# Kernel tuning notes

Hardware: AMD Instinct MI355X
Metric: run time of the kernel (lower is better)

Reference implementation:

```python
import jax, jax.numpy as jnp
import numpy as np

DIM = 8
H1 = 128
H2 = 128
BATCH = 65536


def setup_inputs() -> dict:
    key = jax.random.key(0)
    ks = jax.random.split(key, 9)
    s = lambda k, shape, scale: jax.random.normal(k, shape, dtype=jnp.float32) * scale
    return {
        "X": s(ks[0], (BATCH, 2 * DIM), 1.0),
        "K": s(ks[1], (DIM, DIM), 0.5),
        "D": s(ks[2], (DIM, DIM), 0.5),
        "W0": s(ks[3], (H1, DIM), 1.0 / np.sqrt(DIM)),
        "b0": s(ks[4], (H1,), 0.1),
        "W1": s(ks[5], (H2, H1), 1.0 / np.sqrt(H1)),
        "b1": s(ks[6], (H2,), 0.1),
        "W2": s(ks[7], (1, H2), 1.0 / np.sqrt(H2)),
        "b2": s(ks[8], (1,), 0.1),
    }


def reference(X, K, D, W0, b0, W1, b1, W2, b2):
    dim = K.shape[0]
    x = X[:, :dim]   # position  [B, d]
    v = X[:, dim:]   # velocity  [B, d]

    # Embedding height function f: R^d -> R (MLP with tanh), y = [x, f(x)]
    def f_scalar(xi):
        h = jnp.tanh(W0 @ xi + b0)
        h = jnp.tanh(W1 @ h + b1)
        return (W2 @ h + b2)[0]

    g = jax.vmap(jax.grad(f_scalar))(x)      # grad f   [B, d]
    H = jax.vmap(jax.hessian(f_scalar))(x)   # hess f   [B, d, d]

    eye = jnp.eye(dim, dtype=X.dtype)
    m = eye + g[:, :, None] * g[:, None, :]  # metric I + g g^T  [B, d, d]
    minv = jnp.linalg.inv(m)                 # batched inverse   [B, d, d]

    # linear part: m^{-1} ( -(D v + K x) )
    force = -(v @ D.T + x @ K.T)                      # [B, d]
    lin = jnp.einsum('bqk,bk->bq', minv, force)       # [B, d]

    # geodesic part: Gamma^q_{ij} v^i v^j with Gamma^q_{ij} = (m^{-1} g)_q H_{ij}
    coef = jnp.einsum('bqk,bk->bq', minv, g)          # (m^{-1} grad f)  [B, d]
    hvv = jnp.einsum('bij,bi,bj->b', H, v, v)         # v^T H v          [B]
    quad = coef * hvv[:, None]                        # [B, d]

    return lin - quad
```

## Files before the change

kernel.cpp:

```cpp
#include <hip/hip_runtime.h>
#include <math.h>

#define HDIM 128
#define S 16
#define NT 256
#define ASTR 136
#define PSTR 132

typedef __attribute__((ext_vector_type(8))) short  bf16x8;
typedef __attribute__((ext_vector_type(8))) unsigned short u16x8;
typedef __attribute__((ext_vector_type(4))) float  f32x4;

__device__ __forceinline__ float tanh_fast(float x){
    const float e = __expf(2.0f * x);
    return 1.0f - 2.0f * __builtin_amdgcn_rcpf(e + 1.0f);
}
__device__ __forceinline__ unsigned short bhi(float v){
    return (unsigned short)(__float_as_uint(v) >> 16);
}
__device__ __forceinline__ unsigned short brne(float v){
    unsigned u = __float_as_uint(v);
    return (unsigned short)((u + 0x7FFFu + ((u >> 16) & 1u)) >> 16);
}
__device__ __forceinline__ float bf(unsigned short u){
    return __uint_as_float(((unsigned)u) << 16);
}

__global__ void prep_frags(const float* __restrict__ W1, const float* __restrict__ W0,
                           const float* __restrict__ b0, unsigned short* __restrict__ ws){
    const int t = blockIdx.x * 256 + threadIdx.x;
    if (t < 16384) {
        const int r = t & 7, l = (t >> 3) & 63, tile = t >> 9;
        const int nt = tile >> 2, ks = tile & 3;
        const int m = l >> 4, c = l & 15;
        const int k = ks * 32 + m * 8 + r;
        ws[t]         = brne(W1[(nt * 16 + c) * HDIM + k]);
        ws[32768 + t] = brne(W1[k * HDIM + (nt * 16 + c)]);
    } else if (t < 18432) {
        const int t2 = t - 16384;
        const int r = t2 & 7, l = (t2 >> 3) & 63, ks = t2 >> 9;
        const int m = l >> 4, c = l & 15;
        const int k = ks * 32 + m * 8 + r;
        ws[65536 + t2] = (c < 8) ? brne(W0[k * 8 + c]) : (unsigned short)0;
    } else if (t < 22528) {
        const int t3 = t - 18432;
        const int r = t3 & 7, l = (t3 >> 3) & 63, nt = t3 >> 9;
        const int m = l >> 4, c = l & 15;
        const int k = m * 8 + r;
        const int j = nt * 16 + c;
        float v = 0.f;
        if (k < 8)       v = W0[j * 8 + k];
        else if (k == 8) v = b0[j];
        ws[69632 + t3] = brne(v);
    }
}

__global__ __launch_bounds__(NT)
void dyn_mfma(const float* __restrict__ X, const float* __restrict__ Km,
              const float* __restrict__ Dm, const float* __restrict__ b1,
              const float* __restrict__ W2, const unsigned short* __restrict__ FR,
              float* __restrict__ out)
{
    __shared__ __align__(16) unsigned short act[32 * ASTR];
    __shared__ __align__(16) unsigned int   upk[16 * PSTR];
    __shared__ __align__(16) unsigned short xa_hi[256];
    __shared__ __align__(16) unsigned short xa_lo[256];
    __shared__ float xt[S * 16];
    __shared__ float hvb[2][16];
    __shared__ float hvc[4][16];

    const int tid = threadIdx.x;
    const long base = (long)blockIdx.x * S;

    const int wv = tid >> 6, l = tid & 63;
    const int m = l >> 4, c = l & 15;
    const int mt = wv >> 1, nh = wv & 1;

    {
        xt[tid] = X[base * 16 + tid];
        const int i0 = mt * 128 + l;
        const float xv0 = X[base * 16 + i0];
        const float xv1 = X[base * 16 + i0 + 64];
        unsigned short h0w = bhi(xv0);
        xa_hi[i0] = h0w;           xa_lo[i0] = brne(xv0 - bf(h0w));
        h0w = bhi(xv1);
        xa_hi[i0 + 64] = h0w;      xa_lo[i0 + 64] = brne(xv1 - bf(h0w));
    }

    bf16x8 afh[4];
    #pragma unroll
    for (int n = 0; n < 4; ++n) {
        const int gi = (((nh * 4 + n) * 64) + l) * 8;
        afh[n] = *(const bf16x8*)&FR[69632 + gi];
    }

    f32x4 accA[4];
    #pragma unroll
    for (int n = 0; n < 4; ++n) accA[n] = (f32x4){0.f, 0.f, 0.f, 0.f};
    {
        bf16x8 axh = {0,0,0,0,0,0,0,0}, axl = {0,0,0,0,0,0,0,0};
        if (m == 0) {
            axh = *(const bf16x8*)&xa_hi[(mt * 16 + c) * 8];
            axl = *(const bf16x8*)&xa_lo[(mt * 16 + c) * 8];
        } else if (m == 1) {
            axh[0] = (short)(((c & 1) == 0) ? 0x3F80 : 0);
        }
        #pragma unroll
        for (int n = 0; n < 4; ++n) {
            accA[n] = __builtin_amdgcn_mfma_f32_16x16x32_bf16(axh, afh[n], accA[n], 0, 0, 0);
            accA[n] = __builtin_amdgcn_mfma_f32_16x16x32_bf16(axl, afh[n], accA[n], 0, 0, 0);
        }
    }

    #pragma unroll
    for (int n = 0; n < 4; ++n) {
        const int j = (nh * 4 + n) * 16 + c;
        #pragma unroll
        for (int pr = 0; pr < 2; ++pr) {
            const int s = mt * 8 + 2 * m + pr;
            const float z  = accA[n][2 * pr];
            const float dz = accA[n][2 * pr + 1];
            const float h  = tanh_fast(z);
            const float e  = fmaf(-h, h, 1.f);
            const float dh = e * dz;
            const float a0 = -2.f * h * dh * dz;
            act[(2 * s)     * ASTR + j] = brne(h);
            act[(2 * s + 1) * ASTR + j] = brne(dh);
            upk[s * PSTR + j] = __float_as_uint(a0);
        }
    }

    bf16x8 pbh[2][4];
    #pragma unroll
    for (int ks = 0; ks < 4; ++ks) {
        const int gi = (((nh * 4 + 0) * 4 + ks) * 64 + l) * 8;
        pbh[0][ks] = *(const bf16x8*)&FR[gi];
    }
    float b1v[4], w2v[4];
    #pragma unroll
    for (int n = 0; n < 4; ++n) {
        const int j = (nh * 4 + n) * 16 + c;
        b1v[n] = b1[j];
        w2v[n] = W2[j];
    }
    __syncthreads();

    f32x4 accB[4];
    #pragma unroll
    for (int n = 0; n < 4; ++n) accB[n] = (f32x4){0.f, 0.f, 0.f, 0.f};
    {
        const int arow = mt * 16 + c;
        bf16x8 ah[4];
        #pragma unroll
        for (int ks = 0; ks < 4; ++ks)
            ah[ks] = *(const bf16x8*)&act[arow * ASTR + ks * 32 + m * 8];
        #pragma unroll
        for (int n = 0; n < 4; ++n) {
            const int cur = n & 1;
            if (n < 3) {
                #pragma unroll
                for (int ks = 0; ks < 4; ++ks) {
                    const int gi = (((nh * 4 + n + 1) * 4 + ks) * 64 + l) * 8;
                    pbh[cur ^ 1][ks] = *(const bf16x8*)&FR[gi];
                }
            }
            #pragma unroll
            for (int ks = 0; ks < 4; ++ks)
                accB[n] = __builtin_amdgcn_mfma_f32_16x16x32_bf16(ah[ks], pbh[cur][ks], accB[n], 0, 0, 0);
        }
    }

    const int sA = mt * 8 + 2 * m, sB = sA + 1;
    float u1Av[4], u1Bv[4];
    float hvA = 0.f, hvB = 0.f;
    #pragma unroll
    for (int n = 0; n < 4; ++n) {
        const float zA = accB[n][0] + b1v[n], dzA = accB[n][1];
        const float zB = accB[n][2] + b1v[n], dzB = accB[n][3];
        const float h1A = tanh_fast(zA), e1A = fmaf(-h1A, h1A, 1.f);
        u1Av[n] = w2v[n] * e1A;
        hvA = fmaf(-2.f * w2v[n] * h1A * e1A, dzA * dzA, hvA);
        const float h1B = tanh_fast(zB), e1B = fmaf(-h1B, h1B, 1.f);
        u1Bv[n] = w2v[n] * e1B;
        hvB = fmaf(-2.f * w2v[n] * h1B * e1B, dzB * dzB, hvB);
    }
    #pragma unroll
    for (int mk = 1; mk <= 8; mk <<= 1) {
        hvA += __shfl_xor(hvA, mk);
        hvB += __shfl_xor(hvB, mk);
    }

    bf16x8 cbh[2][4];
    #pragma unroll
    for (int n2 = 0; n2 < 2; ++n2)
        #pragma unroll
        for (int ks = 0; ks < 4; ++ks) {
            const int gi = (((wv * 2 + n2) * 4 + ks) * 64 + l) * 8;
            cbh[n2][ks] = *(const bf16x8*)&FR[32768 + gi];
        }

    __syncthreads();

    #pragma unroll
    for (int n = 0; n < 4; ++n) {
        const int j = (nh * 4 + n) * 16 + c;
        act[(2 * sA + 1) * ASTR + j] = brne(u1Av[n]);
        act[(2 * sB + 1) * ASTR + j] = brne(u1Bv[n]);
    }
    if (c == 0) { hvb[nh][sA] = hvA; hvb[nh][sB] = hvB; }
    __syncthreads();

    f32x4 accC[2];
    accC[0] = (f32x4){0.f, 0.f, 0.f, 0.f};
    accC[1] = (f32x4){0.f, 0.f, 0.f, 0.f};
    {
        const int urow = 2 * c + 1;
        bf16x8 uh4[4];
        #pragma unroll
        for (int ks = 0; ks < 4; ++ks)
            uh4[ks] = *(const bf16x8*)&act[urow * ASTR + ks * 32 + m * 8];
        #pragma unroll
        for (int n2 = 0; n2 < 2; ++n2)
            #pragma unroll
            for (int ks = 0; ks < 4; ++ks)
                accC[n2] = __builtin_amdgcn_mfma_f32_16x16x32_bf16(uh4[ks], cbh[n2][ks], accC[n2], 0, 0, 0);
    }

    {
        float hv1[4] = {0.f, 0.f, 0.f, 0.f};
        #pragma unroll
        for (int n2 = 0; n2 < 2; ++n2) {
            const int i = (wv * 2 + n2) * 16 + c;
            #pragma unroll
            for (int p = 0; p < 4; ++p) {
                const int s = 4 * m + p;
                const float tv = accC[n2][p];
                const float h0 = bf(act[(2 * s) * ASTR + i]);
                const float a0 = __uint_as_float(upk[s * PSTR + i]);
                const float e0 = fmaf(-h0, h0, 1.f);
                const float u0 = e0 * tv;
                hv1[p] = fmaf(a0, tv, hv1[p]);
                upk[s * PSTR + i] = __float_as_uint(u0);
            }
        }
        #pragma unroll
        for (int mk = 1; mk <= 8; mk <<= 1) {
            #pragma unroll
            for (int p = 0; p < 4; ++p) hv1[p] += __shfl_xor(hv1[p], mk);
        }
        if (c == 0) {
            #pragma unroll
            for (int p = 0; p < 4; ++p) hvc[wv][4 * m + p] = hv1[p];
        }
    }

    bf16x8 dbh[4];
    float4 ka, kb, da, db;
    if (wv == 0) {
        #pragma unroll
        for (int ks = 0; ks < 4; ++ks) {
            const int gi = (ks * 64 + l) * 8;
            dbh[ks] = *(const bf16x8*)&FR[65536 + gi];
        }
        const int dd = c & 7;
        ka = ((const float4*)Km)[dd * 2]; kb = ((const float4*)Km)[dd * 2 + 1];
        da = ((const float4*)Dm)[dd * 2]; db = ((const float4*)Dm)[dd * 2 + 1];
    }
    __syncthreads();

    if (wv != 0) return;

    f32x4 accG = (f32x4){0.f, 0.f, 0.f, 0.f};
    #pragma unroll
    for (int ks = 0; ks < 4; ++ks) {
        unsigned u[8];
        *(uint4*)&u[0] = *(const uint4*)&upk[c * PSTR + ks * 32 + m * 8];
        *(uint4*)&u[4] = *(const uint4*)&upk[c * PSTR + ks * 32 + m * 8 + 4];
        bf16x8 ah, al;
        #pragma unroll
        for (int j = 0; j < 8; ++j) {
            const float v = __uint_as_float(u[j]);
            const unsigned short h = bhi(v);
            ah[j] = (short)h;
            al[j] = (short)brne(v - bf(h));
        }
        accG = __builtin_amdgcn_mfma_f32_16x16x32_bf16(ah, dbh[ks], accG, 0, 0, 0);
        accG = __builtin_amdgcn_mfma_f32_16x16x32_bf16(al, dbh[ks], accG, 0, 0, 0);
    }

    {
        #pragma unroll
        for (int p = 0; p < 4; ++p) {
            const int s = 4 * m + p;
            const float g = accG[p];
            const float hvv = hvb[0][s] + hvb[1][s]
                            + hvc[0][s] + hvc[1][s] + hvc[2][s] + hvc[3][s];
            const float* xv = &xt[s * 16];
            float f = ka.x * xv[0];
            f = fmaf(ka.y, xv[1], f);  f = fmaf(ka.z, xv[2], f);  f = fmaf(ka.w, xv[3], f);
            f = fmaf(kb.x, xv[4], f);  f = fmaf(kb.y, xv[5], f);  f = fmaf(kb.z, xv[6], f);
            f = fmaf(kb.w, xv[7], f);
            f = fmaf(da.x, xv[8], f);  f = fmaf(da.y, xv[9], f);  f = fmaf(da.z, xv[10], f);
            f = fmaf(da.w, xv[11], f); f = fmaf(db.x, xv[12], f); f = fmaf(db.y, xv[13], f);
            f = fmaf(db.z, xv[14], f); f = fmaf(db.w, xv[15], f);
            f = -f;
            float pgf = g * f, pgg = g * g;
            #pragma unroll
            for (int mk = 1; mk <= 8; mk <<= 1) {
                pgf += __shfl_xor(pgf, mk);
                pgg += __shfl_xor(pgg, mk);
            }
            const float al_ = (pgf + hvv) * __builtin_amdgcn_rcpf(1.f + pgg);
            if (c < 8)
                out[(base + s) * 8 + c] = fmaf(-g, al_, f);
        }
    }
}

__global__ void dyn_naive(const float* __restrict__ X, const float* __restrict__ Km,
                          const float* __restrict__ Dm, const float* __restrict__ W0,
                          const float* __restrict__ b0, const float* __restrict__ W1,
                          const float* __restrict__ b1, const float* __restrict__ W2,
                          float* __restrict__ out)
{
    const long sidx = (long)blockIdx.x * 64 + threadIdx.x;
    const float* xv = X + sidx * 16;
    float h0[HDIM], dh0[HDIM], a0[HDIM], u1[HDIM];
    for (int k = 0; k < HDIM; ++k) {
        float z = b0[k], dz = 0.f;
        for (int d = 0; d < 8; ++d) { z = fmaf(W0[k*8+d], xv[d], z); dz = fmaf(W0[k*8+d], xv[8+d], dz); }
        const float h = tanhf(z), e = 1.f - h*h;
        h0[k] = h; dh0[k] = e*dz; a0[k] = -2.f*h*e*dz*dz;
    }
    float hvv = 0.f;
    for (int j = 0; j < HDIM; ++j) {
        float z = b1[j], dz = 0.f, cc = 0.f;
        for (int k = 0; k < HDIM; ++k) {
            const float w = W1[j*HDIM+k];
            z = fmaf(w, h0[k], z); dz = fmaf(w, dh0[k], dz); cc = fmaf(w, a0[k], cc);
        }
        const float h = tanhf(z), e = 1.f - h*h;
        u1[j] = W2[j]*e;
        hvv += W2[j]*(e*cc - 2.f*h*e*dz*dz);
    }
    float g[8] = {0,0,0,0,0,0,0,0};
    for (int k = 0; k < HDIM; ++k) {
        float t = 0.f;
        for (int j = 0; j < HDIM; ++j) t = fmaf(u1[j], W1[j*HDIM+k], t);
        const float u0 = (1.f - h0[k]*h0[k]) * t;
        for (int d = 0; d < 8; ++d) g[d] = fmaf(W0[k*8+d], u0, g[d]);
    }
    float fd[8], gf = 0.f, gg = 0.f;
    for (int d = 0; d < 8; ++d) {
        float a = 0.f;
        for (int k = 0; k < 8; ++k) { a = fmaf(Km[d*8+k], xv[k], a); a = fmaf(Dm[d*8+k], xv[8+k], a); }
        fd[d] = -a; gf = fmaf(g[d], fd[d], gf); gg = fmaf(g[d], g[d], gg);
    }
    const float al = (gf + hvv) / (1.f + gg);
    for (int d = 0; d < 8; ++d) out[sidx*8 + d] = fd[d] - g[d]*al;
}

extern "C" void kernel_launch(void* const* d_in, const int* in_sizes, int n_in,
                              void* d_out, int out_size, void* d_ws, size_t ws_size,
                              hipStream_t stream) {
    const float* X  = (const float*)d_in[0];
    const float* Km = (const float*)d_in[1];
    const float* Dm = (const float*)d_in[2];
    const float* W0 = (const float*)d_in[3];
    const float* b0 = (const float*)d_in[4];
    const float* W1 = (const float*)d_in[5];
    const float* b1 = (const float*)d_in[6];
    const float* W2 = (const float*)d_in[7];
    float* out = (float*)d_out;

    const int BATCH = in_sizes[0] / 16;
    if (ws_size >= (size_t)(77824 * sizeof(unsigned short))) {
        unsigned short* FR = (unsigned short*)d_ws;
        prep_frags<<<88, 256, 0, stream>>>(W1, W0, b0, FR);
        dyn_mfma<<<BATCH / S, NT, 0, stream>>>(X, Km, Dm, b1, W2, FR, out);
    } else {
        dyn_naive<<<BATCH / 64, 64, 0, stream>>>(X, Km, Dm, W0, b0, W1, b1, W2, out);
    }
}
```

Baseline: 94.02 us.

## Process 32 samples per block and store intermediates as single bf16

Doubles the samples handled per block from 16 to 32. Each wave loops over two halves, so the fixed per-block costs (fragment loads, syncs, setup) are spread over more work, and two waves now do the final gradient MFMA instead of one. It also stores the a0/u0 intermediates as one rounded bf16 value instead of fp32, which drops the hi/lo split and halves the final-stage MFMAs. This lowers precision of the gradient path, raises LDS use, and halves the number of blocks, which may reduce occupancy and latency hiding.

```diff
diff --git a/kernel.cpp b/kernel.cpp
--- a/kernel.cpp
+++ b/kernel.cpp
@@ -2,13 +2,11 @@
 #include <math.h>
 
 #define HDIM 128
-#define S 16
+#define S 32
 #define NT 256
 #define ASTR 136
-#define PSTR 132
 
 typedef __attribute__((ext_vector_type(8))) short  bf16x8;
-typedef __attribute__((ext_vector_type(8))) unsigned short u16x8;
 typedef __attribute__((ext_vector_type(4))) float  f32x4;
 
 __device__ __forceinline__ float tanh_fast(float x){
@@ -61,13 +59,13 @@
               const float* __restrict__ W2, const unsigned short* __restrict__ FR,
               float* __restrict__ out)
 {
-    __shared__ __align__(16) unsigned short act[32 * ASTR];
-    __shared__ __align__(16) unsigned int   upk[16 * PSTR];
-    __shared__ __align__(16) unsigned short xa_hi[256];
-    __shared__ __align__(16) unsigned short xa_lo[256];
+    __shared__ __align__(16) unsigned short act[64 * ASTR];
+    __shared__ __align__(16) unsigned short upk[32 * ASTR];
+    __shared__ __align__(16) unsigned short xa_hi[512];
+    __shared__ __align__(16) unsigned short xa_lo[512];
     __shared__ float xt[S * 16];
-    __shared__ float hvb[2][16];
-    __shared__ float hvc[4][16];
+    __shared__ float hvb[2][S];
+    __shared__ float hvc[4][S];
 
     const int tid = threadIdx.x;
     const long base = (long)blockIdx.x * S;
@@ -77,14 +75,18 @@
     const int mt = wv >> 1, nh = wv & 1;
 
     {
-        xt[tid] = X[base * 16 + tid];
-        const int i0 = mt * 128 + l;
-        const float xv0 = X[base * 16 + i0];
-        const float xv1 = X[base * 16 + i0 + 64];
-        unsigned short h0w = bhi(xv0);
-        xa_hi[i0] = h0w;           xa_lo[i0] = brne(xv0 - bf(h0w));
-        h0w = bhi(xv1);
-        xa_hi[i0 + 64] = h0w;      xa_lo[i0 + 64] = brne(xv1 - bf(h0w));
+        xt[tid]       = X[base * 16 + tid];
+        xt[256 + tid] = X[base * 16 + 256 + tid];
+        #pragma unroll
+        for (int half = 0; half < 2; ++half) {
+            const int i0 = half * 256 + mt * 128 + l;
+            const float xv0 = X[base * 16 + i0];
+            const float xv1 = X[base * 16 + i0 + 64];
+            unsigned short hw = bhi(xv0);
+            xa_hi[i0] = hw;        xa_lo[i0] = brne(xv0 - bf(hw));
+            hw = bhi(xv1);
+            xa_hi[i0 + 64] = hw;   xa_lo[i0 + 64] = brne(xv1 - bf(hw));
+        }
     }
 
     bf16x8 afh[4];
@@ -94,48 +96,44 @@
         afh[n] = *(const bf16x8*)&FR[69632 + gi];
     }
 
-    f32x4 accA[4];
-    #pragma unroll
-    for (int n = 0; n < 4; ++n) accA[n] = (f32x4){0.f, 0.f, 0.f, 0.f};
-    {
-        bf16x8 axh = {0,0,0,0,0,0,0,0}, axl = {0,0,0,0,0,0,0,0};
-        if (m == 0) {
-            axh = *(const bf16x8*)&xa_hi[(mt * 16 + c) * 8];
-            axl = *(const bf16x8*)&xa_lo[(mt * 16 + c) * 8];
-        } else if (m == 1) {
-            axh[0] = (short)(((c & 1) == 0) ? 0x3F80 : 0);
+    #pragma unroll
+    for (int half = 0; half < 2; ++half) {
+        f32x4 accA[4];
+        #pragma unroll
+        for (int n = 0; n < 4; ++n) accA[n] = (f32x4){0.f, 0.f, 0.f, 0.f};
+        {
+            bf16x8 axh = {0,0,0,0,0,0,0,0}, axl = {0,0,0,0,0,0,0,0};
+            if (m == 0) {
+                axh = *(const bf16x8*)&xa_hi[half * 256 + (mt * 16 + c) * 8];
+                axl = *(const bf16x8*)&xa_lo[half * 256 + (mt * 16 + c) * 8];
+            } else if (m == 1) {
+                axh[0] = (short)(((c & 1) == 0) ? 0x3F80 : 0);
+            }
+            #pragma unroll
+            for (int n = 0; n < 4; ++n) {
+                accA[n] = __builtin_amdgcn_mfma_f32_16x16x32_bf16(axh, afh[n], accA[n], 0, 0, 0);
+                accA[n] = __builtin_amdgcn_mfma_f32_16x16x32_bf16(axl, afh[n], accA[n], 0, 0, 0);
+            }
         }
         #pragma unroll
         for (int n = 0; n < 4; ++n) {
-            accA[n] = __builtin_amdgcn_mfma_f32_16x16x32_bf16(axh, afh[n], accA[n], 0, 0, 0);
-            accA[n] = __builtin_amdgcn_mfma_f32_16x16x32_bf16(axl, afh[n], accA[n], 0, 0, 0);
-        }
-    }
-
-    #pragma unroll
-    for (int n = 0; n < 4; ++n) {
-        const int j = (nh * 4 + n) * 16 + c;
-        #pragma unroll
-        for (int pr = 0; pr < 2; ++pr) {
-            const int s = mt * 8 + 2 * m + pr;
-            const float z  = accA[n][2 * pr];
-            const float dz = accA[n][2 * pr + 1];
-            const float h  = tanh_fast(z);
-            const float e  = fmaf(-h, h, 1.f);
-            const float dh = e * dz;
-            const float a0 = -2.f * h * dh * dz;
-            act[(2 * s)     * ASTR + j] = brne(h);
-            act[(2 * s + 1) * ASTR + j] = brne(dh);
-            upk[s * PSTR + j] = __float_as_uint(a0);
-        }
-    }
-
-    bf16x8 pbh[2][4];
-    #pragma unroll
-    for (int ks = 0; ks < 4; ++ks) {
-        const int gi = (((nh * 4 + 0) * 4 + ks) * 64 + l) * 8;
-        pbh[0][ks] = *(const bf16x8*)&FR[gi];
-    }
+            const int j = (nh * 4 + n) * 16 + c;
+            #pragma unroll
+            for (int pr = 0; pr < 2; ++pr) {
+                const int s = half * 16 + mt * 8 + 2 * m + pr;
+                const float z  = accA[n][2 * pr];
+                const float dz = accA[n][2 * pr + 1];
+                const float h  = tanh_fast(z);
+                const float e  = fmaf(-h, h, 1.f);
+                const float dh = e * dz;
+                const float a0 = -2.f * h * dh * dz;
+                act[(2 * s)     * ASTR + j] = brne(h);
+                act[(2 * s + 1) * ASTR + j] = brne(dh);
+                upk[s * ASTR + j] = brne(a0);
+            }
+        }
+    }
+
     float b1v[4], w2v[4];
     #pragma unroll
     for (int n = 0; n < 4; ++n) {
@@ -145,15 +143,23 @@
     }
     __syncthreads();
 
-    f32x4 accB[4];
-    #pragma unroll
-    for (int n = 0; n < 4; ++n) accB[n] = (f32x4){0.f, 0.f, 0.f, 0.f};
-    {
-        const int arow = mt * 16 + c;
+    float u1r[2][2][4];
+    #pragma unroll
+    for (int half = 0; half < 2; ++half) {
+        const int arow = half * 32 + mt * 16 + c;
         bf16x8 ah[4];
         #pragma unroll
         for (int ks = 0; ks < 4; ++ks)
             ah[ks] = *(const bf16x8*)&act[arow * ASTR + ks * 32 + m * 8];
+        bf16x8 pbh[2][4];
+        #pragma unroll
+        for (int ks = 0; ks < 4; ++ks) {
+            const int gi = (((nh * 4 + 0) * 4 + ks) * 64 + l) * 8;
+            pbh[0][ks] = *(const bf16x8*)&FR[gi];
+        }
+        f32x4 accB[4];
+        #pragma unroll
+        for (int n = 0; n < 4; ++n) accB[n] = (f32x4){0.f, 0.f, 0.f, 0.f};
         #pragma unroll
         for (int n = 0; n < 4; ++n) {
             const int cur = n & 1;
@@ -168,26 +174,25 @@
             for (int ks = 0; ks < 4; ++ks)
                 accB[n] = __builtin_amdgcn_mfma_f32_16x16x32_bf16(ah[ks], pbh[cur][ks], accB[n], 0, 0, 0);
         }
-    }
-
-    const int sA = mt * 8 + 2 * m, sB = sA + 1;
-    float u1Av[4], u1Bv[4];
-    float hvA = 0.f, hvB = 0.f;
-    #pragma unroll
-    for (int n = 0; n < 4; ++n) {
-        const float zA = accB[n][0] + b1v[n], dzA = accB[n][1];
-        const float zB = accB[n][2] + b1v[n], dzB = accB[n][3];
-        const float h1A = tanh_fast(zA), e1A = fmaf(-h1A, h1A, 1.f);
-        u1Av[n] = w2v[n] * e1A;
-        hvA = fmaf(-2.f * w2v[n] * h1A * e1A, dzA * dzA, hvA);
-        const float h1B = tanh_fast(zB), e1B = fmaf(-h1B, h1B, 1.f);
-        u1Bv[n] = w2v[n] * e1B;
-        hvB = fmaf(-2.f * w2v[n] * h1B * e1B, dzB * dzB, hvB);
-    }
-    #pragma unroll
-    for (int mk = 1; mk <= 8; mk <<= 1) {
-        hvA += __shfl_xor(hvA, mk);
-        hvB += __shfl_xor(hvB, mk);
+        const int sA = half * 16 + mt * 8 + 2 * m, sB = sA + 1;
+        float hvA = 0.f, hvB = 0.f;
+        #pragma unroll
+        for (int n = 0; n < 4; ++n) {
+            const float zA = accB[n][0] + b1v[n], dzA = accB[n][1];
+            const float zB = accB[n][2] + b1v[n], dzB = accB[n][3];
+            const float h1A = tanh_fast(zA), e1A = fmaf(-h1A, h1A, 1.f);
+            u1r[half][0][n] = w2v[n] * e1A;
+            hvA = fmaf(-2.f * w2v[n] * h1A * e1A, dzA * dzA, hvA);
+            const float h1B = tanh_fast(zB), e1B = fmaf(-h1B, h1B, 1.f);
+            u1r[half][1][n] = w2v[n] * e1B;
+            hvB = fmaf(-2.f * w2v[n] * h1B * e1B, dzB * dzB, hvB);
+        }
+        #pragma unroll
+        for (int mk = 1; mk <= 8; mk <<= 1) {
+            hvA += __shfl_xor(hvA, mk);
+            hvB += __shfl_xor(hvB, mk);
+        }
+        if (c == 0) { hvb[nh][sA] = hvA; hvb[nh][sB] = hvB; }
     }
 
     bf16x8 cbh[2][4];
@@ -202,45 +207,48 @@
     __syncthreads();
 
     #pragma unroll
-    for (int n = 0; n < 4; ++n) {
-        const int j = (nh * 4 + n) * 16 + c;
-        act[(2 * sA + 1) * ASTR + j] = brne(u1Av[n]);
-        act[(2 * sB + 1) * ASTR + j] = brne(u1Bv[n]);
-    }
-    if (c == 0) { hvb[nh][sA] = hvA; hvb[nh][sB] = hvB; }
+    for (int half = 0; half < 2; ++half) {
+        const int sA = half * 16 + mt * 8 + 2 * m, sB = sA + 1;
+        #pragma unroll
+        for (int n = 0; n < 4; ++n) {
+            const int j = (nh * 4 + n) * 16 + c;
+            act[(2 * sA + 1) * ASTR + j] = brne(u1r[half][0][n]);
+            act[(2 * sB + 1) * ASTR + j] = brne(u1r[half][1][n]);
+        }
+    }
     __syncthreads();
 
-    f32x4 accC[2];
-    accC[0] = (f32x4){0.f, 0.f, 0.f, 0.f};
-    accC[1] = (f32x4){0.f, 0.f, 0.f, 0.f};
-    {
-        const int urow = 2 * c + 1;
-        bf16x8 uh4[4];
-        #pragma unroll
-        for (int ks = 0; ks < 4; ++ks)
-            uh4[ks] = *(const bf16x8*)&act[urow * ASTR + ks * 32 + m * 8];
-        #pragma unroll
-        for (int n2 = 0; n2 < 2; ++n2)
+    #pragma unroll
+    for (int half = 0; half < 2; ++half) {
+        f32x4 accC[2];
+        accC[0] = (f32x4){0.f, 0.f, 0.f, 0.f};
+        accC[1] = (f32x4){0.f, 0.f, 0.f, 0.f};
+        {
+            const int urow = 2 * (half * 16 + c) + 1;
+            bf16x8 uh4[4];
             #pragma unroll
             for (int ks = 0; ks < 4; ++ks)
-                accC[n2] = __builtin_amdgcn_mfma_f32_16x16x32_bf16(uh4[ks], cbh[n2][ks], accC[n2], 0, 0, 0);
-    }
-
-    {
+                uh4[ks] = *(const bf16x8*)&act[urow * ASTR + ks * 32 + m * 8];
+            #pragma unroll
+            for (int n2 = 0; n2 < 2; ++n2)
+                #pragma unroll
+                for (int ks = 0; ks < 4; ++ks)
+                    accC[n2] = __builtin_amdgcn_mfma_f32_16x16x32_bf16(uh4[ks], cbh[n2][ks], accC[n2], 0, 0, 0);
+        }
         float hv1[4] = {0.f, 0.f, 0.f, 0.f};
         #pragma unroll
         for (int n2 = 0; n2 < 2; ++n2) {
             const int i = (wv * 2 + n2) * 16 + c;
             #pragma unroll
             for (int p = 0; p < 4; ++p) {
-                const int s = 4 * m + p;
+                const int s = half * 16 + 4 * m + p;
                 const float tv = accC[n2][p];
                 const float h0 = bf(act[(2 * s) * ASTR + i]);
-                const float a0 = __uint_as_float(upk[s * PSTR + i]);
+                const float a0 = bf(upk[s * ASTR + i]);
                 const float e0 = fmaf(-h0, h0, 1.f);
                 const float u0 = e0 * tv;
                 hv1[p] = fmaf(a0, tv, hv1[p]);
-                upk[s * PSTR + i] = __float_as_uint(u0);
+                upk[s * ASTR + i] = brne(u0);
             }
         }
         #pragma unroll
@@ -250,13 +258,13 @@
         }
         if (c == 0) {
             #pragma unroll
-            for (int p = 0; p < 4; ++p) hvc[wv][4 * m + p] = hv1[p];
+            for (int p = 0; p < 4; ++p) hvc[wv][half * 16 + 4 * m + p] = hv1[p];
         }
     }
 
     bf16x8 dbh[4];
     float4 ka, kb, da, db;
-    if (wv == 0) {
+    if (wv < 2) {
         #pragma unroll
         for (int ks = 0; ks < 4; ++ks) {
             const int gi = (ks * 64 + l) * 8;
@@ -268,30 +276,19 @@
     }
     __syncthreads();
 
-    if (wv != 0) return;
+    if (wv >= 2) return;
 
     f32x4 accG = (f32x4){0.f, 0.f, 0.f, 0.f};
     #pragma unroll
     for (int ks = 0; ks < 4; ++ks) {
-        unsigned u[8];
-        *(uint4*)&u[0] = *(const uint4*)&upk[c * PSTR + ks * 32 + m * 8];
-        *(uint4*)&u[4] = *(const uint4*)&upk[c * PSTR + ks * 32 + m * 8 + 4];
-        bf16x8 ah, al;
-        #pragma unroll
-        for (int j = 0; j < 8; ++j) {
-            const float v = __uint_as_float(u[j]);
-            const unsigned short h = bhi(v);
-            ah[j] = (short)h;
-            al[j] = (short)brne(v - bf(h));
-        }
-        accG = __builtin_amdgcn_mfma_f32_16x16x32_bf16(ah, dbh[ks], accG, 0, 0, 0);
-        accG = __builtin_amdgcn_mfma_f32_16x16x32_bf16(al, dbh[ks], accG, 0, 0, 0);
+        const bf16x8 ua = *(const bf16x8*)&upk[(wv * 16 + c) * ASTR + ks * 32 + m * 8];
+        accG = __builtin_amdgcn_mfma_f32_16x16x32_bf16(ua, dbh[ks], accG, 0, 0, 0);
     }
 
     {
         #pragma unroll
         for (int p = 0; p < 4; ++p) {
-            const int s = 4 * m + p;
+            const int s = wv * 16 + 4 * m + p;
             const float g = accG[p];
             const float hvv = hvb[0][s] + hvb[1][s]
                             + hvc[0][s] + hvc[1][s] + hvc[2][s] + hvc[3][s];
```

Result: no change. 93.37 us (-0.7%).
